# Optimization experiments

Hardware: AMD Instinct MI355X
Metric: run time of the kernel (lower is better)

## Reference

```python
import jax, jax.numpy as jnp
import numpy as np

HEADS = 64
DIM_HEAD = 64
SCALE = DIM_HEAD ** -0.5
EPS = 1e-6


def setup_inputs() -> dict:
    key = jax.random.key(0)
    ks = jax.random.split(key, 6)
    b, s, dim = 2, 4096, 1024
    inner = HEADS * DIM_HEAD  # 4096
    std = 0.02
    return {
        "x": jax.random.normal(ks[0], (b, s, dim), dtype=jnp.float32),
        "Wq": jax.random.normal(ks[1], (dim, inner), dtype=jnp.float32) * std,
        "Wk": jax.random.normal(ks[2], (dim, inner), dtype=jnp.float32) * std,
        "Wv": jax.random.normal(ks[3], (dim, inner), dtype=jnp.float32) * std,
        "Wo": jax.random.normal(ks[4], (inner, dim), dtype=jnp.float32) * std,
        "bo": jnp.zeros((dim,), dtype=jnp.float32),
    }


def reference(x, Wq, Wk, Wv, Wo, bo):
    b, s, dim = x.shape
    h, dh = HEADS, DIM_HEAD
    # projections -> [b, s, h, dh]
    q = (x @ Wq).reshape(b, s, h, dh)
    k = (x @ Wk).reshape(b, s, h, dh)
    v = (x @ Wv).reshape(b, s, h, dh)
    # kernel feature map (relu) + scale on q
    q = jax.nn.relu(q) * SCALE
    k = jax.nn.relu(k)
    # NOTE: faithful to the source, these einsums contract over the HEAD axis
    # per token (i, j index heads; d indexes dim_head).
    kv = jnp.einsum('bsid,bsjd->bsdj', k, v)          # [b, s, dh, h]
    out = jnp.einsum('bsid,bsdj->bsij', q, kv)        # [b, s, h, h]
    q_norm = jnp.einsum('bsid,bsd->bsi', q, k.sum(axis=2))  # [b, s, h]
    out = out / (q_norm[..., None] + EPS)
    out = out.reshape(b, s, h * h)                    # h*h == h*dh since h == dh
    return out @ Wo + bo
```

## Files before the change

kernel.cpp:

```cpp
#include <hip/hip_runtime.h>
#include <hip/hip_bf16.h>
#include <cstdint>

#define M_TOK 8192
#define DIM   1024
#define INNER 4096
#define HEADS 64
#define DH    64
#define QSCALE 0.125f
#define EPS    1e-6f

typedef __hip_bfloat16 bf16;
typedef __bf16 bf16x8_t __attribute__((ext_vector_type(8)));
typedef float f32x4_t __attribute__((ext_vector_type(4)));

__device__ __forceinline__ float bfbits2f(unsigned short u) {
  return __uint_as_float(((unsigned)u) << 16);
}
__device__ __forceinline__ unsigned short f2bfbits(float f) {
  __hip_bfloat16 h = __float2bfloat16(f);
  unsigned short u;
  __builtin_memcpy(&u, &h, 2);
  return u;
}

__device__ __forceinline__ void load_lds16(const void* g, void* l) {
  __builtin_amdgcn_global_load_lds(
      (__attribute__((address_space(1))) void*)g,
      (__attribute__((address_space(3))) void*)l, 16, 0, 0);
}

__device__ __forceinline__ void asm_barrier() {
  asm volatile("s_barrier" ::: "memory");
}

#define LGKM_SB(N) do { \
    asm volatile("s_waitcnt lgkmcnt(" #N ")" ::: "memory"); \
    __builtin_amdgcn_sched_barrier(0); } while (0)

__device__ __forceinline__ void swizzle_xy(int& bx, int& by) {
  const int gx = gridDim.x, gy = gridDim.y;
  const int id  = blockIdx.x + gx * blockIdx.y;
  const int per = gy >> 3;
  const int xcd = id & 7;
  const int s   = id >> 3;
  by = xcd * per + (s % per);
  bx = s / per;
}

__global__ __launch_bounds__(256) void castx_kernel(
    const float* __restrict__ x, unsigned short* __restrict__ xb, int n4)
{
  const int i = blockIdx.x * 256 + threadIdx.x;
  if (i < n4) {
    const float4 v = reinterpret_cast<const float4*>(x)[i];
    ushort4 o;
    o.x = f2bfbits(v.x); o.y = f2bfbits(v.y);
    o.z = f2bfbits(v.z); o.w = f2bfbits(v.w);
    reinterpret_cast<ushort4*>(xb)[i] = o;
  }
}

__global__ __launch_bounds__(256) void tcast_kernel(
    const float* __restrict__ W, unsigned short* __restrict__ Wt, int R, int C)
{
  __shared__ float tile[32][33];
  const int bx = blockIdx.x * 32;
  const int by = blockIdx.y * 32;
  const int tx = threadIdx.x & 31;
  const int ty = threadIdx.x >> 5;
#pragma unroll
  for (int k = 0; k < 4; ++k)
    tile[ty + k * 8][tx] = W[(size_t)(by + ty + k * 8) * C + bx + tx];
  __syncthreads();
#pragma unroll
  for (int k = 0; k < 4; ++k)
    Wt[(size_t)(bx + ty + k * 8) * R + by + tx] = f2bfbits(tile[tx][ty + k * 8]);
}

__global__ __launch_bounds__(256) void tcast_dual_kernel(
    const float* __restrict__ W0, const float* __restrict__ W1,
    unsigned short* __restrict__ Wt, int R, int C)
{
  __shared__ float tile[32][33];
  const float* W = blockIdx.z ? W1 : W0;
  unsigned short* dst = Wt + (size_t)blockIdx.z * R * C;
  const int bx = blockIdx.x * 32;
  const int by = blockIdx.y * 32;
  const int tx = threadIdx.x & 31;
  const int ty = threadIdx.x >> 5;
#pragma unroll
  for (int k = 0; k < 4; ++k)
    tile[ty + k * 8][tx] = W[(size_t)(by + ty + k * 8) * C + bx + tx];
  __syncthreads();
#pragma unroll
  for (int k = 0; k < 4; ++k)
    dst[(size_t)(bx + ty + k * 8) * R + by + tx] = f2bfbits(tile[tx][ty + k * 8]);
}

__device__ __forceinline__ void stage_half(
    const unsigned short* __restrict__ G, unsigned short* L,
    int rowbase, int k0, int K, int h, int tid)
{
#pragma unroll
  for (int j = 0; j < 2; ++j) {
    const int q  = h * 1024 + j * 512 + tid;
    const int r  = q >> 3;
    const int cg = (tid & 7) ^ (r & 7);
    load_lds16(&G[(size_t)(rowbase + r) * K + k0 + cg * 8], &L[q * 8]);
  }
}

__device__ __forceinline__ void read_af4(
    const unsigned short* __restrict__ Ac, bf16x8_t (&af)[8][2],
    int m0, int wm, int l15, int quad)
{
#pragma unroll
  for (int mt = 0; mt < 4; ++mt) {
    const int r = wm + (m0 + mt) * 16 + l15;
#pragma unroll
    for (int kt = 0; kt < 2; ++kt) {
      const int s = (kt * 4 + quad) ^ (r & 7);
      af[m0 + mt][kt] = *reinterpret_cast<const bf16x8_t*>(&Ac[r * 64 + s * 8]);
    }
  }
}

__device__ __forceinline__ void read_bf2(
    const unsigned short* __restrict__ Bc, bf16x8_t (&bfr)[4][2],
    int n0, int wn, int l15, int quad)
{
#pragma unroll
  for (int nt = 0; nt < 2; ++nt) {
    const int r = wn + (n0 + nt) * 16 + l15;
#pragma unroll
    for (int kt = 0; kt < 2; ++kt) {
      const int s = (kt * 4 + quad) ^ (r & 7);
      bfr[n0 + nt][kt] = *reinterpret_cast<const bf16x8_t*>(&Bc[r * 64 + s * 8]);
    }
  }
}

__device__ __forceinline__ void mfma_quad(
    f32x4_t (&acc)[8][4], const bf16x8_t (&af)[8][2],
    const bf16x8_t (&bfr)[4][2], int m0, int n0)
{
  __builtin_amdgcn_s_setprio(1);
#pragma unroll
  for (int mt = m0; mt < m0 + 4; ++mt)
#pragma unroll
    for (int nt = n0; nt < n0 + 2; ++nt) {
      acc[mt][nt] = __builtin_amdgcn_mfma_f32_16x16x32_bf16(
          af[mt][0], bfr[nt][0], acc[mt][nt], 0, 0, 0);
      acc[mt][nt] = __builtin_amdgcn_mfma_f32_16x16x32_bf16(
          af[mt][1], bfr[nt][1], acc[mt][nt], 0, 0, 0);
    }
  __builtin_amdgcn_s_setprio(0);
}

template <int MODE, int DUAL>
__global__ __launch_bounds__(512, 2) void gemm256(
    const unsigned short* __restrict__ A,
    const unsigned short* __restrict__ Bt,
    unsigned short* __restrict__ C0,
    unsigned short* __restrict__ C1,
    int N, int K)
{
  __shared__ __align__(16) unsigned short As[2][256 * 64];
  __shared__ __align__(16) unsigned short Bs[2][256 * 64];

  int bxi, byi;
  swizzle_xy(bxi, byi);
  const int tid  = threadIdx.x;
  const int bm   = byi * 256;
  const int bn   = bxi * 256;
  const int lane = tid & 63;
  const int w    = tid >> 6;
  const int wm   = (w >> 2) * 128;
  const int wn   = (w & 3) * 64;
  const int quad = lane >> 4;
  const int l15  = lane & 15;

  f32x4_t acc[8][4];
#pragma unroll
  for (int mt = 0; mt < 8; ++mt)
#pragma unroll
    for (int nt = 0; nt < 4; ++nt) acc[mt][nt] = (f32x4_t){0.f, 0.f, 0.f, 0.f};

  const int NT = K >> 6;

  bf16x8_t af[8][2], bfr[4][2];

  stage_half(A,  As[0], bm, 0,  K, 0, tid);
  stage_half(A,  As[0], bm, 0,  K, 1, tid);
  stage_half(Bt, Bs[0], bn, 0,  K, 0, tid);
  stage_half(Bt, Bs[0], bn, 0,  K, 1, tid);
  stage_half(A,  As[1], bm, 64, K, 0, tid);
  stage_half(A,  As[1], bm, 64, K, 1, tid);
  asm volatile("s_waitcnt vmcnt(4)" ::: "memory");
  asm_barrier();
  __builtin_amdgcn_sched_barrier(0);
  read_af4(As[0], af, 0, wm, l15, quad);
  read_bf2(Bs[0], bfr, 0, wn, l15, quad);

  for (int T = 0; T < NT; ++T) {
    const int c = T & 1;
    const unsigned short* Ac = As[c];
    const unsigned short* Bc = Bs[c];
    unsigned short* Bnx = Bs[c ^ 1];
    unsigned short* Anx = As[c];
    const int kB = (T + 1) * 64;
    const int kA = (T + 2) * 64;
    const bool pB = (T + 1 < NT);
    const bool pA = (T + 2 < NT);

    read_af4(Ac, af, 4, wm, l15, quad);
    LGKM_SB(8);
    mfma_quad(acc, af, bfr, 0, 0);

    read_bf2(Bc, bfr, 2, wn, l15, quad);
    if (pB) stage_half(Bt, Bnx, bn, kB, K, 0, tid);
    LGKM_SB(4);
    mfma_quad(acc, af, bfr, 4, 0);

    if (pB) stage_half(Bt, Bnx, bn, kB, K, 1, tid);
    if (pA) stage_half(A, Anx, bm, kA, K, 0, tid);
    LGKM_SB(0);
    mfma_quad(acc, af, bfr, 0, 2);

    if (pA) stage_half(A, Anx, bm, kA, K, 1, tid);
    mfma_quad(acc, af, bfr, 4, 2);
    if (T < NT - 2) {
      asm volatile("s_waitcnt vmcnt(4)" ::: "memory");
    } else {
      asm volatile("s_waitcnt vmcnt(0)" ::: "memory");
    }
    asm_barrier();
    __builtin_amdgcn_sched_barrier(0);
    if (T + 1 < NT) {
      read_af4(As[c ^ 1], af, 0, wm, l15, quad);
      read_bf2(Bs[c ^ 1], bfr, 0, wn, l15, quad);
    }
  }

  if (DUAL) {
    const bool isK = (bn < 4096);
    unsigned short* __restrict__ C = isK ? C0 : C1;
    const int bnc = bn & 4095;
#pragma unroll
    for (int mt = 0; mt < 8; ++mt)
#pragma unroll
      for (int i = 0; i < 4; ++i) {
        const size_t rowg = (size_t)(bm + wm + mt * 16 + quad * 4 + i);
#pragma unroll
        for (int nt = 0; nt < 4; ++nt) {
          float v = acc[mt][nt][i];
          if (isK) v = fmaxf(v, 0.f);
          C[rowg * 4096 + bnc + wn + nt * 16 + l15] = f2bfbits(v);
        }
      }
  } else {
#pragma unroll
    for (int mt = 0; mt < 8; ++mt)
#pragma unroll
      for (int i = 0; i < 4; ++i) {
        const size_t rowg = (size_t)(bm + wm + mt * 16 + quad * 4 + i);
#pragma unroll
        for (int nt = 0; nt < 4; ++nt) {
          float v = acc[mt][nt][i];
          if (MODE >= 1) v = fmaxf(v, 0.f);
          if (MODE == 2) v *= QSCALE;
          C0[rowg * (size_t)N + bn + wn + nt * 16 + l15] = f2bfbits(v);
        }
      }
  }
}

__global__ __launch_bounds__(256) void gemm_out_bf16(
    const unsigned short* __restrict__ A,
    const unsigned short* __restrict__ Bt,
    const float* __restrict__ bias,
    float* __restrict__ out, int M, int N, int K)
{
  __shared__ __align__(16) unsigned short As[128 * 64];
  __shared__ __align__(16) unsigned short Bs[64 * 64];

  int bxi, byi;
  swizzle_xy(bxi, byi);
  const int tid  = threadIdx.x;
  const int bm   = byi * 128;
  const int bn   = bxi * 64;
  const int lane = tid & 63;
  const int w    = tid >> 6;
  const int wm   = (w & 1) * 64;
  const int wn   = (w >> 1) * 32;
  const int quad = lane >> 4;
  const int l15  = lane & 15;

  f32x4_t acc[4][2];
#pragma unroll
  for (int mt = 0; mt < 4; ++mt)
#pragma unroll
    for (int nt = 0; nt < 2; ++nt) acc[mt][nt] = (f32x4_t){0.f, 0.f, 0.f, 0.f};

  int qa[4], ra[4], ca[4];
#pragma unroll
  for (int j = 0; j < 4; ++j) {
    qa[j] = tid + 256 * j;
    ra[j] = qa[j] >> 3;
    ca[j] = (qa[j] & 7) ^ (ra[j] & 7);
  }
  int qb[2], rb[2], cb[2];
#pragma unroll
  for (int j = 0; j < 2; ++j) {
    qb[j] = tid + 256 * j;
    rb[j] = qb[j] >> 3;
    cb[j] = (qb[j] & 7) ^ (rb[j] & 7);
  }

  for (int k0 = 0; k0 < K; k0 += 64) {
    __syncthreads();
#pragma unroll
    for (int j = 0; j < 4; ++j)
      load_lds16(&A[(size_t)(bm + ra[j]) * K + k0 + ca[j] * 8], &As[qa[j] * 8]);
#pragma unroll
    for (int j = 0; j < 2; ++j)
      load_lds16(&Bt[(size_t)(bn + rb[j]) * K + k0 + cb[j] * 8], &Bs[qb[j] * 8]);
    __syncthreads();

    bf16x8_t af[4][2], bfr[2][2];
#pragma unroll
    for (int mt = 0; mt < 4; ++mt) {
      const int r = wm + mt * 16 + l15;
#pragma unroll
      for (int kt = 0; kt < 2; ++kt) {
        const int slot = (kt * 4 + quad) ^ (r & 7);
        af[mt][kt] = *reinterpret_cast<const bf16x8_t*>(&As[r * 64 + slot * 8]);
      }
    }
#pragma unroll
    for (int nt = 0; nt < 2; ++nt) {
      const int r = wn + nt * 16 + l15;
#pragma unroll
      for (int kt = 0; kt < 2; ++kt) {
        const int slot = (kt * 4 + quad) ^ (r & 7);
        bfr[nt][kt] = *reinterpret_cast<const bf16x8_t*>(&Bs[r * 64 + slot * 8]);
      }
    }
#pragma unroll
    for (int mt = 0; mt < 4; ++mt)
#pragma unroll
      for (int nt = 0; nt < 2; ++nt) {
        acc[mt][nt] = __builtin_amdgcn_mfma_f32_16x16x32_bf16(
            af[mt][0], bfr[nt][0], acc[mt][nt], 0, 0, 0);
        acc[mt][nt] = __builtin_amdgcn_mfma_f32_16x16x32_bf16(
            af[mt][1], bfr[nt][1], acc[mt][nt], 0, 0, 0);
      }
  }

#pragma unroll
  for (int mt = 0; mt < 4; ++mt)
#pragma unroll
    for (int i = 0; i < 4; ++i) {
      const size_t rowg = (size_t)(bm + wm + mt * 16 + quad * 4 + i);
#pragma unroll
      for (int nt = 0; nt < 2; ++nt) {
        const int colg = bn + wn + nt * 16 + l15;
        out[rowg * N + colg] = acc[mt][nt][i] + bias[colg];
      }
    }
}

__global__ __launch_bounds__(256) void ksum_kernel(
    const unsigned short* __restrict__ Kb, float* __restrict__ ks)
{
  const int t = blockIdx.x * 4 + (threadIdx.x >> 6);
  const int j = threadIdx.x & 63;
  const uint4* row = reinterpret_cast<const uint4*>(Kb + (size_t)t * INNER);
  float s[8] = {0.f, 0.f, 0.f, 0.f, 0.f, 0.f, 0.f, 0.f};
#pragma unroll
  for (int m = 0; m < 8; ++m) {
    const uint4 u = row[j + 64 * m];
    s[0] += __uint_as_float((u.x & 0xFFFFu) << 16);
    s[1] += __uint_as_float(u.x & 0xFFFF0000u);
    s[2] += __uint_as_float((u.y & 0xFFFFu) << 16);
    s[3] += __uint_as_float(u.y & 0xFFFF0000u);
    s[4] += __uint_as_float((u.z & 0xFFFFu) << 16);
    s[5] += __uint_as_float(u.z & 0xFFFF0000u);
    s[6] += __uint_as_float((u.w & 0xFFFFu) << 16);
    s[7] += __uint_as_float(u.w & 0xFFFF0000u);
  }
#pragma unroll
  for (int off = 8; off < 64; off <<= 1)
#pragma unroll
    for (int e = 0; e < 8; ++e) s[e] += __shfl_xor(s[e], off, 64);
  if (j < 8) {
    float4* dst = reinterpret_cast<float4*>(ks + t * 64 + j * 8);
    float4 lo, hi;
    lo.x = s[0]; lo.y = s[1]; lo.z = s[2]; lo.w = s[3];
    hi.x = s[4]; hi.y = s[5]; hi.z = s[6]; hi.w = s[7];
    dst[0] = lo; dst[1] = hi;
  }
}

__global__ __launch_bounds__(256) void attn_mfma(
    const unsigned short* __restrict__ Qb, const unsigned short* __restrict__ Vb,
    const float* __restrict__ ksum, unsigned short* __restrict__ Ab)
{
  const int t    = blockIdx.x * 4 + (threadIdx.x >> 6);
  const int lane = threadIdx.x & 63;
  const int l15  = lane & 15;
  const int quad = lane >> 4;
  const size_t base = (size_t)t * INNER;

  union VU { bf16x8_t v; unsigned short u[8]; };

  float ksv[2][8];
#pragma unroll
  for (int kt = 0; kt < 2; ++kt) {
    const float4* p = reinterpret_cast<const float4*>(ksum + t * 64 + kt * 32 + quad * 8);
    const float4 a = p[0], b = p[1];
    ksv[kt][0] = a.x; ksv[kt][1] = a.y; ksv[kt][2] = a.z; ksv[kt][3] = a.w;
    ksv[kt][4] = b.x; ksv[kt][5] = b.y; ksv[kt][6] = b.z; ksv[kt][7] = b.w;
  }

  bf16x8_t vs[4][2];
#pragma unroll
  for (int nt = 0; nt < 4; ++nt)
#pragma unroll
    for (int kt = 0; kt < 2; ++kt) {
      VU vr, vo;
      vr.v = *reinterpret_cast<const bf16x8_t*>(
          Vb + base + (size_t)(nt * 16 + l15) * 64 + kt * 32 + quad * 8);
#pragma unroll
      for (int j = 0; j < 8; ++j)
        vo.u[j] = f2bfbits(bfbits2f(vr.u[j]) * ksv[kt][j]);
      vs[nt][kt] = vo.v;
    }

  bf16x8_t qf[4][2];
  float qn[4] = {0.f, 0.f, 0.f, 0.f};
#pragma unroll
  for (int mt = 0; mt < 4; ++mt)
#pragma unroll
    for (int kt = 0; kt < 2; ++kt) {
      VU qr;
      qr.v = *reinterpret_cast<const bf16x8_t*>(
          Qb + base + (size_t)(mt * 16 + l15) * 64 + kt * 32 + quad * 8);
      qf[mt][kt] = qr.v;
#pragma unroll
      for (int j = 0; j < 8; ++j)
        qn[mt] += bfbits2f(qr.u[j]) * ksv[kt][j];
    }
#pragma unroll
  for (int mt = 0; mt < 4; ++mt) {
    qn[mt] += __shfl_xor(qn[mt], 16, 64);
    qn[mt] += __shfl_xor(qn[mt], 32, 64);
  }

  f32x4_t acc[4][4];
#pragma unroll
  for (int mt = 0; mt < 4; ++mt)
#pragma unroll
    for (int nt = 0; nt < 4; ++nt) acc[mt][nt] = (f32x4_t){0.f, 0.f, 0.f, 0.f};

#pragma unroll
  for (int mt = 0; mt < 4; ++mt)
#pragma unroll
    for (int nt = 0; nt < 4; ++nt) {
      acc[mt][nt] = __builtin_amdgcn_mfma_f32_16x16x32_bf16(
          qf[mt][0], vs[nt][0], acc[mt][nt], 0, 0, 0);
      acc[mt][nt] = __builtin_amdgcn_mfma_f32_16x16x32_bf16(
          qf[mt][1], vs[nt][1], acc[mt][nt], 0, 0, 0);
    }

#pragma unroll
  for (int mt = 0; mt < 4; ++mt)
#pragma unroll
    for (int i = 0; i < 4; ++i) {
      const float inv = 1.f / (__shfl(qn[mt], quad * 4 + i, 64) + EPS);
      const size_t roff = base + (size_t)(mt * 16 + quad * 4 + i) * 64;
#pragma unroll
      for (int nt = 0; nt < 4; ++nt)
        Ab[roff + nt * 16 + l15] = f2bfbits(acc[mt][nt][i] * inv);
    }
}

extern "C" void kernel_launch(void* const* d_in, const int* in_sizes, int n_in,
                              void* d_out, int out_size, void* d_ws, size_t ws_size,
                              hipStream_t stream)
{
  const float* x  = (const float*)d_in[0];
  const float* Wq = (const float*)d_in[1];
  const float* Wk = (const float*)d_in[2];
  const float* Wv = (const float*)d_in[3];
  const float* Wo = (const float*)d_in[4];
  const float* bo = (const float*)d_in[5];
  float* out = (float*)d_out;

  uint8_t* ws = (uint8_t*)d_ws;
  const size_t HALF = (size_t)M_TOK * INNER * sizeof(bf16);
  unsigned short* KQA = (unsigned short*)ws;
  unsigned short* Vb  = (unsigned short*)(ws + HALF);
  float* ks           = (float*)(ws + 2 * HALF);

  unsigned short* Xb   = (unsigned short*)d_out;
  unsigned short* WtKV = (unsigned short*)((uint8_t*)d_out + (16u << 20));
  unsigned short* WqT  = WtKV;
  unsigned short* Wot  = Vb;

  const dim3 blk(256);
  const dim3 blk512(512);

  castx_kernel<<<dim3(M_TOK * DIM / 4 / 256), blk, 0, stream>>>(
      x, Xb, M_TOK * DIM / 4);

  tcast_dual_kernel<<<dim3(INNER / 32, DIM / 32, 2), blk, 0, stream>>>(
      Wk, Wv, WtKV, DIM, INNER);

  gemm256<0, 1><<<dim3(2 * INNER / 256, M_TOK / 256), blk512, 0, stream>>>(
      Xb, WtKV, KQA, Vb, 2 * INNER, DIM);

  ksum_kernel<<<dim3(M_TOK / 4), blk, 0, stream>>>(KQA, ks);

  tcast_kernel<<<dim3(INNER / 32, DIM / 32), blk, 0, stream>>>(
      Wq, WqT, DIM, INNER);

  gemm256<2, 0><<<dim3(INNER / 256, M_TOK / 256), blk512, 0, stream>>>(
      Xb, WqT, KQA, nullptr, INNER, DIM);

  attn_mfma<<<dim3(M_TOK / 4), blk, 0, stream>>>(KQA, Vb, ks, KQA);

  tcast_kernel<<<dim3(DIM / 32, INNER / 32), blk, 0, stream>>>(
      Wo, Wot, INNER, DIM);

  gemm_out_bf16<<<dim3(DIM / 64, M_TOK / 128), blk, 0, stream>>>(
      KQA, Wot, bo, out, M_TOK, DIM, INNER);
}
```

Measured before the change: 465.1 us.

## Replace 256-tile GEMMs with 128x128 triple-buffered BK=32 GEMMs

The 256x256, 512-thread projection GEMM is replaced by a 128x128, 256-thread kernel with BK=32 and a three-stage LDS ring, which gives smaller tiles and more resident blocks per CU. The output GEMM moves from a 128x64 single-buffered tile to the same 128x128 triple-buffered pipeline. The aim is better occupancy and better overlap of loads with MFMA work. In exchange, the projection GEMMs get less operand reuse per block and have half the K-depth per barrier.

```diff
diff --git a/kernel.cpp b/kernel.cpp
--- a/kernel.cpp
+++ b/kernel.cpp
@@ -98,138 +98,94 @@
     dst[(size_t)(bx + ty + k * 8) * R + by + tx] = f2bfbits(tile[tx][ty + k * 8]);
 }
 
-__device__ __forceinline__ void stage_half(
+__device__ __forceinline__ void stage32(
     const unsigned short* __restrict__ G, unsigned short* L,
-    int rowbase, int k0, int K, int h, int tid)
+    int rowbase, int k0, int K, int tid)
 {
 #pragma unroll
   for (int j = 0; j < 2; ++j) {
-    const int q  = h * 1024 + j * 512 + tid;
-    const int r  = q >> 3;
-    const int cg = (tid & 7) ^ (r & 7);
+    const int q  = j * 256 + tid;
+    const int r  = q >> 2;
+    const int s  = q & 3;
+    const int cg = s ^ (r & 3) ^ ((r >> 2) & 3);
     load_lds16(&G[(size_t)(rowbase + r) * K + k0 + cg * 8], &L[q * 8]);
   }
 }
 
-__device__ __forceinline__ void read_af4(
-    const unsigned short* __restrict__ Ac, bf16x8_t (&af)[8][2],
-    int m0, int wm, int l15, int quad)
-{
-#pragma unroll
-  for (int mt = 0; mt < 4; ++mt) {
-    const int r = wm + (m0 + mt) * 16 + l15;
-#pragma unroll
-    for (int kt = 0; kt < 2; ++kt) {
-      const int s = (kt * 4 + quad) ^ (r & 7);
-      af[m0 + mt][kt] = *reinterpret_cast<const bf16x8_t*>(&Ac[r * 64 + s * 8]);
-    }
-  }
-}
-
-__device__ __forceinline__ void read_bf2(
-    const unsigned short* __restrict__ Bc, bf16x8_t (&bfr)[4][2],
-    int n0, int wn, int l15, int quad)
-{
-#pragma unroll
-  for (int nt = 0; nt < 2; ++nt) {
-    const int r = wn + (n0 + nt) * 16 + l15;
-#pragma unroll
-    for (int kt = 0; kt < 2; ++kt) {
-      const int s = (kt * 4 + quad) ^ (r & 7);
-      bfr[n0 + nt][kt] = *reinterpret_cast<const bf16x8_t*>(&Bc[r * 64 + s * 8]);
-    }
-  }
-}
-
-__device__ __forceinline__ void mfma_quad(
-    f32x4_t (&acc)[8][4], const bf16x8_t (&af)[8][2],
-    const bf16x8_t (&bfr)[4][2], int m0, int n0)
-{
-  __builtin_amdgcn_s_setprio(1);
-#pragma unroll
-  for (int mt = m0; mt < m0 + 4; ++mt)
-#pragma unroll
-    for (int nt = n0; nt < n0 + 2; ++nt) {
-      acc[mt][nt] = __builtin_amdgcn_mfma_f32_16x16x32_bf16(
-          af[mt][0], bfr[nt][0], acc[mt][nt], 0, 0, 0);
-      acc[mt][nt] = __builtin_amdgcn_mfma_f32_16x16x32_bf16(
-          af[mt][1], bfr[nt][1], acc[mt][nt], 0, 0, 0);
-    }
-  __builtin_amdgcn_s_setprio(0);
-}
-
 template <int MODE, int DUAL>
-__global__ __launch_bounds__(512, 2) void gemm256(
+__global__ __launch_bounds__(256, 3) void gemm128(
     const unsigned short* __restrict__ A,
     const unsigned short* __restrict__ Bt,
     unsigned short* __restrict__ C0,
     unsigned short* __restrict__ C1,
     int N, int K)
 {
-  __shared__ __align__(16) unsigned short As[2][256 * 64];
-  __shared__ __align__(16) unsigned short Bs[2][256 * 64];
+  __shared__ __align__(16) unsigned short As[3][128 * 32];
+  __shared__ __align__(16) unsigned short Bs[3][128 * 32];
 
   int bxi, byi;
   swizzle_xy(bxi, byi);
   const int tid  = threadIdx.x;
-  const int bm   = byi * 256;
-  const int bn   = bxi * 256;
+  const int bm   = byi * 128;
+  const int bn   = bxi * 128;
   const int lane = tid & 63;
   const int w    = tid >> 6;
-  const int wm   = (w >> 2) * 128;
-  const int wn   = (w & 3) * 64;
+  const int wm   = (w & 1) * 64;
+  const int wn   = (w >> 1) * 64;
   const int quad = lane >> 4;
   const int l15  = lane & 15;
 
-  f32x4_t acc[8][4];
-#pragma unroll
-  for (int mt = 0; mt < 8; ++mt)
+  f32x4_t acc[4][4];
+#pragma unroll
+  for (int mt = 0; mt < 4; ++mt)
 #pragma unroll
     for (int nt = 0; nt < 4; ++nt) acc[mt][nt] = (f32x4_t){0.f, 0.f, 0.f, 0.f};
 
-  const int NT = K >> 6;
-
-  bf16x8_t af[8][2], bfr[4][2];
-
-  stage_half(A,  As[0], bm, 0,  K, 0, tid);
-  stage_half(A,  As[0], bm, 0,  K, 1, tid);
-  stage_half(Bt, Bs[0], bn, 0,  K, 0, tid);
-  stage_half(Bt, Bs[0], bn, 0,  K, 1, tid);
-  stage_half(A,  As[1], bm, 64, K, 0, tid);
-  stage_half(A,  As[1], bm, 64, K, 1, tid);
+  const int NT = K >> 5;
+
+  stage32(A,  As[0], bm, 0,  K, tid);
+  stage32(Bt, Bs[0], bn, 0,  K, tid);
+  stage32(A,  As[1], bm, 32, K, tid);
+  stage32(Bt, Bs[1], bn, 32, K, tid);
   asm volatile("s_waitcnt vmcnt(4)" ::: "memory");
   asm_barrier();
   __builtin_amdgcn_sched_barrier(0);
-  read_af4(As[0], af, 0, wm, l15, quad);
-  read_bf2(Bs[0], bfr, 0, wn, l15, quad);
-
+
+  bf16x8_t af[4], bfr[4];
+
+  int c = 0;
+  int cs = 2;
   for (int T = 0; T < NT; ++T) {
-    const int c = T & 1;
     const unsigned short* Ac = As[c];
     const unsigned short* Bc = Bs[c];
-    unsigned short* Bnx = Bs[c ^ 1];
-    unsigned short* Anx = As[c];
-    const int kB = (T + 1) * 64;
-    const int kA = (T + 2) * 64;
-    const bool pB = (T + 1 < NT);
     const bool pA = (T + 2 < NT);
-
-    read_af4(Ac, af, 4, wm, l15, quad);
-    LGKM_SB(8);
-    mfma_quad(acc, af, bfr, 0, 0);
-
-    read_bf2(Bc, bfr, 2, wn, l15, quad);
-    if (pB) stage_half(Bt, Bnx, bn, kB, K, 0, tid);
-    LGKM_SB(4);
-    mfma_quad(acc, af, bfr, 4, 0);
-
-    if (pB) stage_half(Bt, Bnx, bn, kB, K, 1, tid);
-    if (pA) stage_half(A, Anx, bm, kA, K, 0, tid);
+    const int kN = (T + 2) * 32;
+
+#pragma unroll
+    for (int mt = 0; mt < 4; ++mt) {
+      const int r = wm + mt * 16 + l15;
+      const int s = quad ^ (r & 3) ^ ((r >> 2) & 3);
+      af[mt] = *reinterpret_cast<const bf16x8_t*>(&Ac[r * 32 + s * 8]);
+    }
+#pragma unroll
+    for (int nt = 0; nt < 4; ++nt) {
+      const int r = wn + nt * 16 + l15;
+      const int s = quad ^ (r & 3) ^ ((r >> 2) & 3);
+      bfr[nt] = *reinterpret_cast<const bf16x8_t*>(&Bc[r * 32 + s * 8]);
+    }
     LGKM_SB(0);
-    mfma_quad(acc, af, bfr, 0, 2);
-
-    if (pA) stage_half(A, Anx, bm, kA, K, 1, tid);
-    mfma_quad(acc, af, bfr, 4, 2);
+    if (pA) {
+      stage32(A,  As[cs], bm, kN, K, tid);
+      stage32(Bt, Bs[cs], bn, kN, K, tid);
+    }
+    __builtin_amdgcn_s_setprio(1);
+#pragma unroll
+    for (int mt = 0; mt < 4; ++mt)
+#pragma unroll
+      for (int nt = 0; nt < 4; ++nt)
+        acc[mt][nt] = __builtin_amdgcn_mfma_f32_16x16x32_bf16(
+            af[mt], bfr[nt], acc[mt][nt], 0, 0, 0);
+    __builtin_amdgcn_s_setprio(0);
     if (T < NT - 2) {
       asm volatile("s_waitcnt vmcnt(4)" ::: "memory");
     } else {
@@ -237,10 +193,8 @@
     }
     asm_barrier();
     __builtin_amdgcn_sched_barrier(0);
-    if (T + 1 < NT) {
-      read_af4(As[c ^ 1], af, 0, wm, l15, quad);
-      read_bf2(Bs[c ^ 1], bfr, 0, wn, l15, quad);
-    }
+    c  = (c  == 2) ? 0 : c + 1;
+    cs = (cs == 2) ? 0 : cs + 1;
   }
 
   if (DUAL) {
@@ -248,7 +202,7 @@
     unsigned short* __restrict__ C = isK ? C0 : C1;
     const int bnc = bn & 4095;
 #pragma unroll
-    for (int mt = 0; mt < 8; ++mt)
+    for (int mt = 0; mt < 4; ++mt)
 #pragma unroll
       for (int i = 0; i < 4; ++i) {
         const size_t rowg = (size_t)(bm + wm + mt * 16 + quad * 4 + i);
@@ -261,7 +215,7 @@
       }
   } else {
 #pragma unroll
-    for (int mt = 0; mt < 8; ++mt)
+    for (int mt = 0; mt < 4; ++mt)
 #pragma unroll
       for (int i = 0; i < 4; ++i) {
         const size_t rowg = (size_t)(bm + wm + mt * 16 + quad * 4 + i);
@@ -276,86 +230,86 @@
   }
 }
 
-__global__ __launch_bounds__(256) void gemm_out_bf16(
+__global__ __launch_bounds__(256, 3) void gemm_out128(
     const unsigned short* __restrict__ A,
     const unsigned short* __restrict__ Bt,
     const float* __restrict__ bias,
-    float* __restrict__ out, int M, int N, int K)
-{
-  __shared__ __align__(16) unsigned short As[128 * 64];
-  __shared__ __align__(16) unsigned short Bs[64 * 64];
+    float* __restrict__ out, int N, int K)
+{
+  __shared__ __align__(16) unsigned short As[3][128 * 32];
+  __shared__ __align__(16) unsigned short Bs[3][128 * 32];
 
   int bxi, byi;
   swizzle_xy(bxi, byi);
   const int tid  = threadIdx.x;
   const int bm   = byi * 128;
-  const int bn   = bxi * 64;
+  const int bn   = bxi * 128;
   const int lane = tid & 63;
   const int w    = tid >> 6;
   const int wm   = (w & 1) * 64;
-  const int wn   = (w >> 1) * 32;
+  const int wn   = (w >> 1) * 64;
   const int quad = lane >> 4;
   const int l15  = lane & 15;
 
-  f32x4_t acc[4][2];
-#pragma unroll
-  for (int mt = 0; mt < 4; ++mt)
-#pragma unroll
-    for (int nt = 0; nt < 2; ++nt) acc[mt][nt] = (f32x4_t){0.f, 0.f, 0.f, 0.f};
-
-  int qa[4], ra[4], ca[4];
-#pragma unroll
-  for (int j = 0; j < 4; ++j) {
-    qa[j] = tid + 256 * j;
-    ra[j] = qa[j] >> 3;
-    ca[j] = (qa[j] & 7) ^ (ra[j] & 7);
-  }
-  int qb[2], rb[2], cb[2];
-#pragma unroll
-  for (int j = 0; j < 2; ++j) {
-    qb[j] = tid + 256 * j;
-    rb[j] = qb[j] >> 3;
-    cb[j] = (qb[j] & 7) ^ (rb[j] & 7);
-  }
-
-  for (int k0 = 0; k0 < K; k0 += 64) {
-    __syncthreads();
-#pragma unroll
-    for (int j = 0; j < 4; ++j)
-      load_lds16(&A[(size_t)(bm + ra[j]) * K + k0 + ca[j] * 8], &As[qa[j] * 8]);
-#pragma unroll
-    for (int j = 0; j < 2; ++j)
-      load_lds16(&Bt[(size_t)(bn + rb[j]) * K + k0 + cb[j] * 8], &Bs[qb[j] * 8]);
-    __syncthreads();
-
-    bf16x8_t af[4][2], bfr[2][2];
+  f32x4_t acc[4][4];
+#pragma unroll
+  for (int mt = 0; mt < 4; ++mt)
+#pragma unroll
+    for (int nt = 0; nt < 4; ++nt) acc[mt][nt] = (f32x4_t){0.f, 0.f, 0.f, 0.f};
+
+  const int NT = K >> 5;
+
+  stage32(A,  As[0], bm, 0,  K, tid);
+  stage32(Bt, Bs[0], bn, 0,  K, tid);
+  stage32(A,  As[1], bm, 32, K, tid);
+  stage32(Bt, Bs[1], bn, 32, K, tid);
+  asm volatile("s_waitcnt vmcnt(4)" ::: "memory");
+  asm_barrier();
+  __builtin_amdgcn_sched_barrier(0);
+
+  bf16x8_t af[4], bfr[4];
+
+  int c = 0, cs = 2;
+  for (int T = 0; T < NT; ++T) {
+    const unsigned short* Ac = As[c];
+    const unsigned short* Bc = Bs[c];
+    const bool pA = (T + 2 < NT);
+    const int kN = (T + 2) * 32;
+
 #pragma unroll
     for (int mt = 0; mt < 4; ++mt) {
       const int r = wm + mt * 16 + l15;
-#pragma unroll
-      for (int kt = 0; kt < 2; ++kt) {
-        const int slot = (kt * 4 + quad) ^ (r & 7);
-        af[mt][kt] = *reinterpret_cast<const bf16x8_t*>(&As[r * 64 + slot * 8]);
-      }
-    }
-#pragma unroll
-    for (int nt = 0; nt < 2; ++nt) {
+      const int s = quad ^ (r & 3) ^ ((r >> 2) & 3);
+      af[mt] = *reinterpret_cast<const bf16x8_t*>(&Ac[r * 32 + s * 8]);
+    }
+#pragma unroll
+    for (int nt = 0; nt < 4; ++nt) {
       const int r = wn + nt * 16 + l15;
-#pragma unroll
-      for (int kt = 0; kt < 2; ++kt) {
-        const int slot = (kt * 4 + quad) ^ (r & 7);
-        bfr[nt][kt] = *reinterpret_cast<const bf16x8_t*>(&Bs[r * 64 + slot * 8]);
-      }
-    }
+      const int s = quad ^ (r & 3) ^ ((r >> 2) & 3);
+      bfr[nt] = *reinterpret_cast<const bf16x8_t*>(&Bc[r * 32 + s * 8]);
+    }
+    LGKM_SB(0);
+    if (pA) {
+      stage32(A,  As[cs], bm, kN, K, tid);
+      stage32(Bt, Bs[cs], bn, kN, K, tid);
+    }
+    __builtin_amdgcn_s_setprio(1);
 #pragma unroll
     for (int mt = 0; mt < 4; ++mt)
 #pragma unroll
-      for (int nt = 0; nt < 2; ++nt) {
+      for (int nt = 0; nt < 4; ++nt)
         acc[mt][nt] = __builtin_amdgcn_mfma_f32_16x16x32_bf16(
-            af[mt][0], bfr[nt][0], acc[mt][nt], 0, 0, 0);
-        acc[mt][nt] = __builtin_amdgcn_mfma_f32_16x16x32_bf16(
-            af[mt][1], bfr[nt][1], acc[mt][nt], 0, 0, 0);
-      }
+            af[mt], bfr[nt], acc[mt][nt], 0, 0, 0);
+    __builtin_amdgcn_s_setprio(0);
+    if (T < NT - 2) {
+      asm volatile("s_waitcnt vmcnt(4)" ::: "memory");
+    } else {
+      asm volatile("s_waitcnt vmcnt(0)" ::: "memory");
+    }
+    asm_barrier();
+    __builtin_amdgcn_sched_barrier(0);
+    c  = (c  == 2) ? 0 : c + 1;
+    cs = (cs == 2) ? 0 : cs + 1;
   }
 
 #pragma unroll
@@ -364,7 +318,7 @@
     for (int i = 0; i < 4; ++i) {
       const size_t rowg = (size_t)(bm + wm + mt * 16 + quad * 4 + i);
 #pragma unroll
-      for (int nt = 0; nt < 2; ++nt) {
+      for (int nt = 0; nt < 4; ++nt) {
         const int colg = bn + wn + nt * 16 + l15;
         out[rowg * N + colg] = acc[mt][nt][i] + bias[colg];
       }
@@ -510,7 +464,6 @@
   unsigned short* Wot  = Vb;
 
   const dim3 blk(256);
-  const dim3 blk512(512);
 
   castx_kernel<<<dim3(M_TOK * DIM / 4 / 256), blk, 0, stream>>>(
       x, Xb, M_TOK * DIM / 4);
@@ -518,7 +471,7 @@
   tcast_dual_kernel<<<dim3(INNER / 32, DIM / 32, 2), blk, 0, stream>>>(
       Wk, Wv, WtKV, DIM, INNER);
 
-  gemm256<0, 1><<<dim3(2 * INNER / 256, M_TOK / 256), blk512, 0, stream>>>(
+  gemm128<0, 1><<<dim3(2 * INNER / 128, M_TOK / 128), blk, 0, stream>>>(
       Xb, WtKV, KQA, Vb, 2 * INNER, DIM);
 
   ksum_kernel<<<dim3(M_TOK / 4), blk, 0, stream>>>(KQA, ks);
@@ -526,7 +479,7 @@
   tcast_kernel<<<dim3(INNER / 32, DIM / 32), blk, 0, stream>>>(
       Wq, WqT, DIM, INNER);
 
-  gemm256<2, 0><<<dim3(INNER / 256, M_TOK / 256), blk512, 0, stream>>>(
+  gemm128<2, 0><<<dim3(INNER / 128, M_TOK / 128), blk, 0, stream>>>(
       Xb, WqT, KQA, nullptr, INNER, DIM);
 
   attn_mfma<<<dim3(M_TOK / 4), blk, 0, stream>>>(KQA, Vb, ks, KQA);
@@ -534,6 +487,6 @@
   tcast_kernel<<<dim3(DIM / 32, INNER / 32), blk, 0, stream>>>(
       Wo, Wot, INNER, DIM);
 
-  gemm_out_bf16<<<dim3(DIM / 64, M_TOK / 128), blk, 0, stream>>>(
-      KQA, Wot, bo, out, M_TOK, DIM, INNER);
-}
+  gemm_out128<<<dim3(DIM / 128, M_TOK / 128), blk, 0, stream>>>(
+      KQA, Wot, bo, out, DIM, INNER);
+}
```

Result: slower. 504.0 us (+8.4%).
